# Optimization experiments

Measured on AMD Instinct MI355X. Metric: run time of the kernel, lower is better.

## Reference

```python
import jax, jax.numpy as jnp
import numpy as np

HEADS = 8
DIM = 512
DH = DIM // HEADS          # 64
M = DIM // 2               # 256 landmarks
PINV_ITERS = 6
KER = 33                   # residual depthwise conv kernel size
EPS_LN = 1e-5


def setup_inputs() -> dict:
    key = jax.random.key(0)
    ks = jax.random.split(key, 5)
    b, n, d = 4, 8192, DIM
    inner = HEADS * DH
    x = jax.random.normal(ks[0], (b, n, d), jnp.float32)
    gamma = jnp.ones((d,), jnp.float32)
    beta = jnp.zeros((d,), jnp.float32)
    w_qkv = jax.random.normal(ks[1], (d, inner * 3), jnp.float32) * (d ** -0.5)
    res_kernel = jax.random.normal(ks[2], (HEADS, 1, KER, 1), jnp.float32) * 0.1  # depthwise (groups=heads)
    w_out = jax.random.normal(ks[3], (inner, d), jnp.float32) * (inner ** -0.5)
    b_out = jnp.zeros((d,), jnp.float32)
    return dict(x=x, gamma=gamma, beta=beta, w_qkv=w_qkv,
                res_kernel=res_kernel, w_out=w_out, b_out=b_out)


def _moore_penrose_pinv(x, iters=PINV_ITERS):
    # iterative Moore-Penrose pseudo-inverse (Razavi et al.), matches lucidrains impl
    I = jnp.eye(x.shape[-1], dtype=x.dtype)
    denom = jnp.max(jnp.sum(jnp.abs(x), axis=-1)) * jnp.max(jnp.sum(jnp.abs(x), axis=-2))
    z = jnp.swapaxes(x, -1, -2) / denom
    for _ in range(iters):
        xz = x @ z
        z = 0.25 * z @ (13.0 * I - xz @ (15.0 * I - xz @ (7.0 * I - xz)))
    return z


def _forward(x, gamma, beta, w_qkv, res_kernel, w_out, b_out):
    b, n, d = x.shape
    # pre-norm (LayerNorm)
    mu = jnp.mean(x, axis=-1, keepdims=True)
    var = jnp.var(x, axis=-1, keepdims=True)
    normed = (x - mu) / jnp.sqrt(var + EPS_LN) * gamma + beta
    # left-pad so sequence divisible by num_landmarks (static, 0 here)
    pad = (-n) % M
    xp = jnp.pad(normed, ((0, 0), (pad, 0), (0, 0)))
    N = n + pad
    qkv = xp @ w_qkv                                    # [b,N,3*h*dh]
    q, k, v = jnp.split(qkv, 3, axis=-1)
    to_heads = lambda t: t.reshape(b, N, HEADS, DH).transpose(0, 2, 1, 3)  # [b,h,N,dh]
    q = to_heads(q) * (DH ** -0.5)
    k = to_heads(k)
    v = to_heads(v)
    l = N // M
    q_l = q.reshape(b, HEADS, M, l, DH).mean(axis=3)    # [b,h,m,dh] landmarks
    k_l = k.reshape(b, HEADS, M, l, DH).mean(axis=3)
    attn1 = jax.nn.softmax(jnp.einsum('bhnd,bhmd->bhnm', q, k_l), axis=-1)   # [b,h,N,m]
    attn2 = jax.nn.softmax(jnp.einsum('bhmd,bhld->bhml', q_l, k_l), axis=-1) # [b,h,m,m]
    attn3 = jax.nn.softmax(jnp.einsum('bhmd,bhnd->bhmn', q_l, k), axis=-1)   # [b,h,m,N]
    out = attn1 @ (_moore_penrose_pinv(attn2) @ (attn3 @ v))                 # [b,h,N,dh]
    # depthwise conv residual over v (channels = heads)
    conv = jax.lax.conv_general_dilated(
        v, res_kernel, window_strides=(1, 1),
        padding=((KER // 2, KER // 2), (0, 0)),
        feature_group_count=HEADS,
        dimension_numbers=('NCHW', 'OIHW', 'NCHW'))
    out = out + conv
    out = out.transpose(0, 2, 1, 3).reshape(b, N, HEADS * DH)
    out = out @ w_out + b_out                           # to_out (dropout = identity at eval)
    out = out[:, -n:]                                   # drop left padding
    return x + out                                      # TransLayer residual


def reference(x, gamma, beta, w_qkv, res_kernel, w_out, b_out):
    return _forward(x, gamma, beta, w_qkv, res_kernel, w_out, b_out)
```

## Files before the change

kernel.cpp:

```cpp
#include <hip/hip_runtime.h>
#include <hip/hip_bf16.h>

#define B_ 4
#define N_ 8192
#define D_ 512
#define H_ 8
#define DH_ 64
#define M_ 256
#define LCH 32
#define KER_ 33
#define NSPLIT 16
#define CS (N_/NSPLIT)

typedef __hip_bfloat16 bf16;
typedef __attribute__((ext_vector_type(8))) short short8;
typedef __attribute__((ext_vector_type(4))) short short4v;
typedef __attribute__((ext_vector_type(4))) float f32x4;

__device__ __forceinline__ float bf2f(bf16 h){ return __bfloat162float(h); }
__device__ __forceinline__ bf16 f2bf(float f){ return __float2bfloat16(f); }
__device__ __forceinline__ f32x4 mfma16(short8 a, short8 b, f32x4 c){
  return __builtin_amdgcn_mfma_f32_16x16x32_bf16(a, b, c, 0, 0, 0);
}

__global__ __launch_bounds__(256) void k_layernorm(const float* __restrict__ x,
    const float* __restrict__ gamma, const float* __restrict__ beta,
    bf16* __restrict__ xn){
  int row = blockIdx.x;
  const float* xr = x + (size_t)row * D_;
  bf16* o = xn + (size_t)row * D_;
  int t = threadIdx.x;
  float v0 = xr[t], v1 = xr[t+256];
  float s = v0+v1, ss = v0*v0 + v1*v1;
  __shared__ float sh[8];
  for (int off=32; off; off>>=1){ s += __shfl_xor(s,off); ss += __shfl_xor(ss,off); }
  int lane = t&63, wid = t>>6;
  if (lane==0){ sh[wid] = s; sh[wid+4] = ss; }
  __syncthreads();
  float S  = sh[0]+sh[1]+sh[2]+sh[3];
  float SS = sh[4]+sh[5]+sh[6]+sh[7];
  float mu = S*(1.f/D_);
  float var = SS*(1.f/D_) - mu*mu;
  float rs = rsqrtf(var + 1e-5f);
  o[t]     = f2bf((v0-mu)*rs*gamma[t]     + beta[t]);
  o[t+256] = f2bf((v1-mu)*rs*gamma[t+256] + beta[t+256]);
}

__global__ __launch_bounds__(256) void k_wt2(const float* __restrict__ W1, bf16* __restrict__ WT1,
    const float* __restrict__ W2, bf16* __restrict__ WT2o){
  int bx = blockIdx.x;
  const float* W; bf16* WT; int C, cx;
  if (bx < 24){ W = W1; WT = WT1; C = 1536; cx = bx; }
  else        { W = W2; WT = WT2o; C = 512;  cx = bx - 24; }
  int c0 = cx*64, r0 = blockIdx.y*64;
  __shared__ float tile[64][65];
  int t = threadIdx.x;
  for (int i=t;i<4096;i+=256){ int r=i>>6, c=i&63; tile[r][c] = W[(size_t)(r0+r)*C + c0+c]; }
  __syncthreads();
  for (int i=t;i<512;i+=256){
    int c=i>>3, rg=i&7;
    short8 o;
    #pragma unroll
    for (int j=0;j<8;j++) ((bf16*)&o)[j] = f2bf(tile[rg*8+j][c]);
    *(short8*)&WT[(size_t)(c0+c)*512 + r0 + rg*8] = o;
  }
}

__global__ __launch_bounds__(256, 2) void k_mm_qkv4(const bf16* __restrict__ A, const bf16* __restrict__ WT,
    bf16* __restrict__ qbuf, bf16* __restrict__ kbuf, bf16* __restrict__ vbuf,
    bf16* __restrict__ vT, bf16* __restrict__ qlb, bf16* __restrict__ klb){
  __shared__ __align__(16) bf16 smem[3*128*72];
  bf16 (*As)[72]  = (bf16(*)[72])smem;
  bf16 (*Bs0)[72] = (bf16(*)[72])(smem + 128*72);
  bf16 (*Bs1)[72] = (bf16(*)[72])(smem + 2*128*72);
  bf16 (*ebuf)[136] = (bf16(*)[136])smem;
  int t = threadIdx.x;
  int w = t>>6, lane = t&63, qd = lane>>4, n = lane&15;
  int wm = w>>1, wn = w&1;
  int r0 = blockIdx.y*128, c0 = blockIdx.x*256;
  f32x4 acc[2][4][4];
  #pragma unroll
  for (int cb=0;cb<2;cb++)
    #pragma unroll
    for (int i=0;i<4;i++)
      #pragma unroll
      for (int j=0;j<4;j++) acc[cb][i][j] = (f32x4){0.f,0.f,0.f,0.f};
  int srow = t>>3, skc = t&7;
  for (int k0=0; k0<512; k0+=64){
    #pragma unroll
    for (int ch=0; ch<4; ch++){
      int m = ch*32 + srow;
      *(short8*)&As[m][skc*8]  = *(const short8*)&A [(size_t)(r0+m)*512 + k0 + skc*8];
      *(short8*)&Bs0[m][skc*8] = *(const short8*)&WT[(size_t)(c0+m)*512 + k0 + skc*8];
      *(short8*)&Bs1[m][skc*8] = *(const short8*)&WT[(size_t)(c0+128+m)*512 + k0 + skc*8];
    }
    __syncthreads();
    #pragma unroll
    for (int ksub=0; ksub<2; ksub++){
      short8 af[4];
      #pragma unroll
      for (int i=0;i<4;i++) af[i] = *(const short8*)&As[wm*64+i*16+n][ksub*32+qd*8];
      #pragma unroll
      for (int cb=0; cb<2; cb++){
        bf16 (*Bsc)[72] = cb ? Bs1 : Bs0;
        short8 bfr[4];
        #pragma unroll
        for (int j=0;j<4;j++) bfr[j] = *(const short8*)&Bsc[wn*64+j*16+n][ksub*32+qd*8];
        #pragma unroll
        for (int i=0;i<4;i++)
          #pragma unroll
          for (int j=0;j<4;j++) acc[cb][i][j] = mfma16(af[i], bfr[j], acc[cb][i][j]);
      }
    }
    __syncthreads();
  }
  int part = c0 >> 9;
  bf16* dst = (part==0)? qbuf : (part==1)? kbuf : vbuf;
  float scale = (part==0)? 0.125f : 1.f;
  int b = r0 >> 13, nn = r0 & 8191;
  #pragma unroll
  for (int cb=0; cb<2; cb++){
    __syncthreads();
    #pragma unroll
    for (int i=0;i<4;i++)
      #pragma unroll
      for (int j=0;j<4;j++)
        #pragma unroll
        for (int rg=0; rg<4; rg++)
          ebuf[wm*64+i*16+qd*4+rg][wn*64+j*16+n] = f2bf(acc[cb][i][j][rg]*scale);
    __syncthreads();
    #pragma unroll
    for (int rep=0; rep<8; rep++){
      int unit = rep*256 + t;
      int row = unit >> 4, ch = unit & 15;
      int col = c0 + cb*128 + ch*8;
      int cc = col & 511, h = cc>>6, dh = cc&63;
      *(short8*)&dst[(((size_t)(b*H_+h))*N_ + nn + row)*DH_ + dh] = *(const short8*)&ebuf[row][ch*8];
    }
    if (part < 2){
      bf16* lt = (part==0) ? qlb : klb;
      #pragma unroll
      for (int rep=0; rep<2; rep++){
        int oi = rep*256 + t;
        int chunk = oi >> 7, col = oi & 127;
        float sum = 0.f;
        #pragma unroll
        for (int rr=0; rr<32; rr++) sum += bf2f(ebuf[chunk*32+rr][col]);
        int m = (nn >> 5) + chunk;
        int cc = (c0 + cb*128 + col) & 511;
        int h = cc >> 6, dh = cc & 63;
        lt[(((size_t)(b*H_+h))*M_ + m)*DH_ + dh] = f2bf(sum * (1.f/LCH));
      }
    } else {
      __syncthreads();
      #pragma unroll
      for (int i=0;i<4;i++)
        #pragma unroll
        for (int j=0;j<4;j++){
          short4v tv;
          #pragma unroll
          for (int rg=0; rg<4; rg++) ((bf16*)&tv)[rg] = f2bf(acc[cb][i][j][rg]);
          *(short4v*)&ebuf[wn*64+j*16+n][wm*64+i*16+qd*4] = tv;
        }
      __syncthreads();
      #pragma unroll
      for (int rep=0; rep<8; rep++){
        int unit = rep*256 + t;
        int col = unit >> 4, ch = unit & 15;
        int cc = (c0 + cb*128 + col) & 511;
        int h = cc >> 6, dh = cc & 63;
        *(short8*)&vT[(((size_t)(b*H_+h))*DH_ + dh)*N_ + nn + ch*8] = *(const short8*)&ebuf[col][ch*8];
      }
    }
  }
}

__global__ __launch_bounds__(256) void k_attn2(const bf16* __restrict__ ql, const bf16* __restrict__ kl,
    float* __restrict__ A2, bf16* __restrict__ A2b){
  int bhm = blockIdx.x;
  int bh = bhm >> 8, m = bhm & 255;
  int t = threadIdx.x;
  __shared__ float qrow[64];
  __shared__ float sh[4];
  if (t < 64) qrow[t] = bf2f(ql[((size_t)bh*M_ + m)*DH_ + t]);
  __syncthreads();
  const bf16* krow = kl + ((size_t)bh*M_ + t)*DH_;
  float s = 0.f;
  #pragma unroll
  for (int i=0;i<64;i++) s += qrow[i]*bf2f(krow[i]);
  float e = __expf(s);
  float sum = e;
  for (int off=32; off; off>>=1) sum += __shfl_xor(sum, off);
  if ((t&63)==0) sh[t>>6] = sum;
  __syncthreads();
  sum = sh[0]+sh[1]+sh[2]+sh[3];
  float r = e/sum;
  A2[((size_t)bh*M_ + m)*M_ + t] = r;
  A2b[((size_t)bh*M_ + m)*M_ + t] = f2bf(r);
}

__global__ __launch_bounds__(256) void k_pinv_init(const float* __restrict__ A2, bf16* __restrict__ Z){
  int bh = blockIdx.x;
  int t = threadIdx.x;
  const float* Ab = A2 + (size_t)bh*M_*M_;
  bf16* Zb = Z + (size_t)bh*M_*M_;
  float cs=0.f;
  for (int r=0;r<M_;r++) cs += Ab[(size_t)r*M_ + t];
  __shared__ float sh[4];
  float v = cs;
  for (int off=32; off; off>>=1) v = fmaxf(v, __shfl_xor(v, off));
  if ((t&63)==0) sh[t>>6] = v;
  __syncthreads();
  float maxc = fmaxf(fmaxf(sh[0],sh[1]), fmaxf(sh[2],sh[3]));
  float inv = 1.f/maxc;
  for (int r=0;r<M_;r++) Zb[(size_t)r*M_ + t] = f2bf(Ab[(size_t)t*M_ + r]*inv);
}

__global__ __launch_bounds__(256) void k_gemm_pmb(bf16* __restrict__ C, const bf16* __restrict__ A,
    const bf16* __restrict__ Bm, float bDiag, int bNeg, float cDiag, int cNeg, float cScale){
  int bh = blockIdx.y;
  int tm = blockIdx.x >> 2, tn = blockIdx.x & 3;
  const bf16* Ab = A  + (size_t)bh*65536;
  const bf16* Bb = Bm + (size_t)bh*65536;
  bf16* Cb = C + (size_t)bh*65536;
  __shared__ __align__(16) bf16 Ah[64][136];
  __shared__ __align__(16) bf16 Bh[64][136];
  int t = threadIdx.x;
  int w = t>>6, lane = t&63, qd = lane>>4, n = lane&15;
  int wm = w>>1, wn = w&1;
  int r0 = tm*64, c0 = tn*64;
  f32x4 acc[2][2];
  #pragma unroll
  for (int i=0;i<2;i++)
    #pragma unroll
    for (int j=0;j<2;j++) acc[i][j] = (f32x4){0.f,0.f,0.f,0.f};
  int arow = t>>2, akc = (t&3)*32;
  int bkrow = t>>1, bcc = (t&1)*32;
  for (int k0=0; k0<256; k0+=128){
    #pragma unroll
    for (int vv=0; vv<4; vv++)
      *(short8*)&Ah[arow][akc+vv*8] = *(const short8*)&Ab[(size_t)(r0+arow)*256 + k0+akc+vv*8];
    int kr = k0 + bkrow;
    #pragma unroll
    for (int vv=0; vv<4; vv++){
      short8 vb = *(const short8*)&Bb[(size_t)kr*256 + c0 + bcc + vv*8];
      if (bNeg){
        #pragma unroll
        for (int j=0;j<8;j++){
          float x = (kr == (c0 + bcc + vv*8 + j) ? bDiag : 0.f) - bf2f(((bf16*)&vb)[j]);
          Bh[bcc+vv*8+j][bkrow] = f2bf(x);
        }
      } else {
        #pragma unroll
        for (int j=0;j<8;j++) Bh[bcc+vv*8+j][bkrow] = ((bf16*)&vb)[j];
      }
    }
    __syncthreads();
    #pragma unroll
    for (int ksub=0; ksub<4; ksub++){
      short8 afh[2], bfh[2];
      #pragma unroll
      for (int i=0;i<2;i++) afh[i] = *(const short8*)&Ah[wm*32+i*16+n][ksub*32+qd*8];
      #pragma unroll
      for (int j=0;j<2;j++) bfh[j] = *(const short8*)&Bh[wn*32+j*16+n][ksub*32+qd*8];
      #pragma unroll
      for (int i=0;i<2;i++)
        #pragma unroll
        for (int j=0;j<2;j++) acc[i][j] = mfma16(afh[i], bfh[j], acc[i][j]);
    }
    __syncthreads();
  }
  #pragma unroll
  for (int i=0;i<2;i++){
    #pragma unroll
    for (int j=0;j<2;j++){
      int cidx = c0 + wn*32 + j*16 + n;
      #pragma unroll
      for (int rg=0; rg<4; rg++){
        int r = r0 + wm*32 + i*16 + qd*4 + rg;
        float r_ = acc[i][j][rg];
        if (cNeg) r_ = ((r==cidx)? cDiag : 0.f) - r_;
        Cb[(size_t)r*256 + cidx] = f2bf(r_*cScale);
      }
    }
  }
}

__global__ __launch_bounds__(256) void k_gemm_pm(float* __restrict__ C, const void* __restrict__ Av,
    const void* __restrict__ Bv, float bDiag, int bNeg, float cDiag, int cNeg, float cScale,
    int aBf, int bBf){
  int bh = blockIdx.y;
  int tm = blockIdx.x >> 2, tn = blockIdx.x & 3;
  const float* Af = (const float*)Av; const bf16* A16 = (const bf16*)Av;
  const float* Bf = (const float*)Bv; const bf16* B16 = (const bf16*)Bv;
  float* Cb = C + (size_t)bh*65536;
  __shared__ __align__(16) bf16 Ah[64][72];
  __shared__ __align__(16) bf16 Al[64][72];
  __shared__ __align__(16) bf16 Bh[64][72];
  __shared__ __align__(16) bf16 Bl[64][72];
  int t = threadIdx.x;
  int w = t>>6, lane = t&63, qd = lane>>4, n = lane&15;
  int wm = w>>1, wn = w&1;
  int r0 = tm*64, c0 = tn*64;
  f32x4 acc[2][2];
  #pragma unroll
  for (int i=0;i<2;i++)
    #pragma unroll
    for (int j=0;j<2;j++) acc[i][j] = (f32x4){0.f,0.f,0.f,0.f};
  int srow = t>>3, skc = t&7;
  for (int k0=0; k0<256; k0+=64){
    #pragma unroll
    for (int ch=0; ch<2; ch++){
      int m = ch*32 + srow;
      if (aBf){
        *(short8*)&Ah[m][skc*8] = *(const short8*)&A16[(size_t)bh*65536 + (size_t)(r0+m)*256 + k0 + skc*8];
      } else {
        short8 vh, vl;
        const float* ap = &Af[(size_t)bh*65536 + (size_t)(r0+m)*256 + k0 + skc*8];
        #pragma unroll
        for (int j=0;j<8;j++){
          float x = ap[j];
          bf16 h = f2bf(x);
          ((bf16*)&vh)[j] = h;
          ((bf16*)&vl)[j] = f2bf(x - bf2f(h));
        }
        *(short8*)&Ah[m][skc*8] = vh;
        *(short8*)&Al[m][skc*8] = vl;
      }
      int kr = k0 + m;
      if (bBf){
        short8 vb = *(const short8*)&B16[(size_t)bh*65536 + (size_t)(k0+m)*256 + c0 + skc*8];
        #pragma unroll
        for (int j=0;j<8;j++) Bh[skc*8+j][m] = ((bf16*)&vb)[j];
      } else {
        const float* bp = &Bf[(size_t)bh*65536 + (size_t)(k0+m)*256 + c0 + skc*8];
        #pragma unroll
        for (int j=0;j<8;j++){
          float x = bp[j];
          if (bNeg) x = (kr == (c0 + skc*8 + j) ? bDiag : 0.f) - x;
          bf16 h = f2bf(x);
          Bh[skc*8+j][m] = h;
          Bl[skc*8+j][m] = f2bf(x - bf2f(h));
        }
      }
    }
    __syncthreads();
    #pragma unroll
    for (int ksub=0; ksub<2; ksub++){
      short8 afh[2], afl[2], bfh[2], bfl[2];
      #pragma unroll
      for (int i=0;i<2;i++){
        afh[i] = *(const short8*)&Ah[wm*32+i*16+n][ksub*32+qd*8];
        if (!aBf) afl[i] = *(const short8*)&Al[wm*32+i*16+n][ksub*32+qd*8];
      }
      #pragma unroll
      for (int j=0;j<2;j++){
        bfh[j] = *(const short8*)&Bh[wn*32+j*16+n][ksub*32+qd*8];
        if (!bBf) bfl[j] = *(const short8*)&Bl[wn*32+j*16+n][ksub*32+qd*8];
      }
      #pragma unroll
      for (int i=0;i<2;i++)
        #pragma unroll
        for (int j=0;j<2;j++){
          if (!aBf) acc[i][j] = mfma16(afl[i], bfh[j], acc[i][j]);
          if (!bBf) acc[i][j] = mfma16(afh[i], bfl[j], acc[i][j]);
          acc[i][j] = mfma16(afh[i], bfh[j], acc[i][j]);
        }
    }
    __syncthreads();
  }
  #pragma unroll
  for (int i=0;i<2;i++){
    #pragma unroll
    for (int j=0;j<2;j++){
      int cidx = c0 + wn*32 + j*16 + n;
      #pragma unroll
      for (int rg=0; rg<4; rg++){
        int r = r0 + wm*32 + i*16 + qd*4 + rg;
        float r_ = acc[i][j][rg];
        if (cNeg) r_ = ((r==cidx)? cDiag : 0.f) - r_;
        Cb[(size_t)r*256 + cidx] = r_*cScale;
      }
    }
  }
}

__global__ __launch_bounds__(256) void k_gemm_z2(bf16* __restrict__ z2t, const float* __restrict__ A,
    const bf16* __restrict__ Bm){
  int bh = blockIdx.y;
  int tm = blockIdx.x;
  const float* Ab = A  + (size_t)bh*65536;
  const bf16* Bb = Bm + (size_t)bh*M_*DH_;
  __shared__ float As[16][68];
  __shared__ float Bs[16][64];
  int t = threadIdx.x, tx = t&15, ty = t>>4;
  int r0 = tm*64;
  float acc[4][4] = {};
  for (int k0=0;k0<256;k0+=16){
    for (int i=t;i<1024;i+=256){
      int m=i>>4, kq=i&15;
      As[kq][m] = Ab[(size_t)(r0+m)*256 + k0+kq];
      int nn=i&63, k2=i>>6;
      Bs[k2][nn] = bf2f(Bb[(size_t)(k0+k2)*64 + nn]);
    }
    __syncthreads();
    #pragma unroll
    for (int kq=0;kq<16;kq++){
      float a0[4], b0[4];
      #pragma unroll
      for (int i=0;i<4;i++) a0[i] = As[kq][ty*4+i];
      #pragma unroll
      for (int j=0;j<4;j++) b0[j] = Bs[kq][tx*4+j];
      #pragma unroll
      for (int i=0;i<4;i++)
        #pragma unroll
        for (int j=0;j<4;j++) acc[i][j] += a0[i]*b0[j];
    }
    __syncthreads();
  }
  #pragma unroll
  for (int i=0;i<4;i++){
    int r = r0+ty*4+i;
    #pragma unroll
    for (int j=0;j<4;j++)
      z2t[(size_t)bh*16384 + (size_t)(tx*4+j)*256 + r] = f2bf(acc[i][j]);
  }
}

__global__ __launch_bounds__(256, 2) void k_flash_split(const bf16* __restrict__ Q,
    const bf16* __restrict__ K, const bf16* __restrict__ VT,
    float* __restrict__ OP, float* __restrict__ LP){
  int bh = blockIdx.y;
  int sp = blockIdx.x;
  int t = threadIdx.x, w = t>>6, lane = t&63, qd = lane>>4, n = lane&15;
  int r0 = w*64;
  const size_t Qoff = ((size_t)bh*M_ + r0)*DH_;
  const size_t Koff = ((size_t)bh*N_ + (size_t)sp*CS)*DH_;
  const size_t Voff = (size_t)bh*DH_*N_ + (size_t)sp*CS;
  __shared__ __align__(16) bf16 pbuf[4][4][16][72];
  short8 aq[4][2];
  #pragma unroll
  for (int rt=0; rt<4; rt++){
    aq[rt][0] = *(const short8*)&Q[Qoff + (size_t)(rt*16+n)*DH_ + qd*8];
    aq[rt][1] = *(const short8*)&Q[Qoff + (size_t)(rt*16+n)*DH_ + 32 + qd*8];
  }
  f32x4 o[4][4];
  float lrun[4][4];
  #pragma unroll
  for (int rt=0; rt<4; rt++){
    #pragma unroll
    for (int j=0;j<4;j++){ o[rt][j] = (f32x4){0.f,0.f,0.f,0.f}; lrun[rt][j] = 0.f; }
  }
  for (int tl=0; tl<CS/64; ++tl){
    const bf16* kp = K + Koff + (size_t)(tl*64)*DH_;
    short8 kb[4][2];
    #pragma unroll
    for (int cg=0; cg<4; cg++){
      kb[cg][0] = *(const short8*)&kp[(size_t)(cg*16+n)*DH_ + qd*8];
      kb[cg][1] = *(const short8*)&kp[(size_t)(cg*16+n)*DH_ + 32 + qd*8];
    }
    #pragma unroll
    for (int rt=0; rt<4; rt++){
      f32x4 s[4];
      #pragma unroll
      for (int cg=0; cg<4; cg++){
        f32x4 z = (f32x4){0.f,0.f,0.f,0.f};
        z = mfma16(aq[rt][0], kb[cg][0], z);
        z = mfma16(aq[rt][1], kb[cg][1], z);
        s[cg] = z;
      }
      #pragma unroll
      for (int rg=0; rg<4; rg++){
        float p0 = __expf(s[0][rg]), p1 = __expf(s[1][rg]);
        float p2 = __expf(s[2][rg]), p3 = __expf(s[3][rg]);
        float ts = p0+p1+p2+p3;
        ts += __shfl_xor(ts,1); ts += __shfl_xor(ts,2);
        ts += __shfl_xor(ts,4); ts += __shfl_xor(ts,8);
        lrun[rt][rg] += ts;
        pbuf[w][rt][qd*4+rg][n]    = f2bf(p0);
        pbuf[w][rt][qd*4+rg][16+n] = f2bf(p1);
        pbuf[w][rt][qd*4+rg][32+n] = f2bf(p2);
        pbuf[w][rt][qd*4+rg][48+n] = f2bf(p3);
      }
    }
    const bf16* vp = VT + Voff + tl*64 + qd*8;
    short8 vb[4][2];
    #pragma unroll
    for (int dg=0; dg<4; dg++){
      vb[dg][0] = *(const short8*)&vp[(size_t)(dg*16+n)*N_];
      vb[dg][1] = *(const short8*)&vp[(size_t)(dg*16+n)*N_ + 32];
    }
    #pragma unroll
    for (int rt=0; rt<4; rt++){
      short8 ap0 = *(const short8*)&pbuf[w][rt][n][qd*8];
      short8 ap1 = *(const short8*)&pbuf[w][rt][n][32+qd*8];
      #pragma unroll
      for (int dg=0; dg<4; dg++){
        o[rt][dg] = mfma16(ap0, vb[dg][0], o[rt][dg]);
        o[rt][dg] = mfma16(ap1, vb[dg][1], o[rt][dg]);
      }
    }
  }
  size_t base = ((size_t)sp*(B_*H_) + bh)*M_;
  #pragma unroll
  for (int rt=0; rt<4; rt++){
    #pragma unroll
    for (int rg=0; rg<4; rg++){
      int row = r0 + rt*16 + qd*4 + rg;
      if (n==0) LP[base+row] = lrun[rt][rg];
      #pragma unroll
      for (int dg=0; dg<4; dg++)
        OP[(base+row)*DH_ + dg*16 + n] = o[rt][dg][rg];
    }
  }
}

__global__ __launch_bounds__(256) void k_flash_merge(const float* __restrict__ OP,
    const float* __restrict__ LP, bf16* __restrict__ O){
  int bh = blockIdx.y;
  int r = blockIdx.x*4 + (threadIdx.x>>6);
  int dh = threadIdx.x & 63;
  float acc = 0.f, den = 0.f;
  for (int s=0; s<NSPLIT; s++){
    size_t base = ((size_t)s*(B_*H_) + bh)*M_ + r;
    den += LP[base];
    acc += OP[base*DH_ + dh];
  }
  O[((size_t)bh*M_ + r)*DH_ + dh] = f2bf(acc/den);
}

__global__ __launch_bounds__(256, 2) void k_flash_w3(const bf16* __restrict__ Q,
    const bf16* __restrict__ K, const bf16* __restrict__ VT, bf16* __restrict__ O){
  int bh = blockIdx.y;
  int t = threadIdx.x, w = t>>6, lane = t&63, qd = lane>>4, n = lane&15;
  int r0 = blockIdx.x*256 + w*64;
  const size_t Qoff = ((size_t)bh*N_ + r0)*DH_;
  const size_t Koff = (size_t)bh*M_*DH_;
  const size_t Voff = (size_t)bh*DH_*M_;
  __shared__ __align__(16) bf16 pbuf[4][4][16][72];
  short8 aq[4][2];
  #pragma unroll
  for (int rt=0; rt<4; rt++){
    aq[rt][0] = *(const short8*)&Q[Qoff + (size_t)(rt*16+n)*DH_ + qd*8];
    aq[rt][1] = *(const short8*)&Q[Qoff + (size_t)(rt*16+n)*DH_ + 32 + qd*8];
  }
  f32x4 o[4][4];
  float lrun[4][4];
  #pragma unroll
  for (int rt=0; rt<4; rt++){
    #pragma unroll
    for (int j=0;j<4;j++){ o[rt][j] = (f32x4){0.f,0.f,0.f,0.f}; lrun[rt][j] = 0.f; }
  }
  #pragma unroll
  for (int tl=0; tl<4; ++tl){
    const bf16* kp = K + Koff + (size_t)(tl*64)*DH_;
    short8 kb[4][2];
    #pragma unroll
    for (int cg=0; cg<4; cg++){
      kb[cg][0] = *(const short8*)&kp[(size_t)(cg*16+n)*DH_ + qd*8];
      kb[cg][1] = *(const short8*)&kp[(size_t)(cg*16+n)*DH_ + 32 + qd*8];
    }
    #pragma unroll
    for (int rt=0; rt<4; rt++){
      f32x4 s[4];
      #pragma unroll
      for (int cg=0; cg<4; cg++){
        f32x4 z = (f32x4){0.f,0.f,0.f,0.f};
        z = mfma16(aq[rt][0], kb[cg][0], z);
        z = mfma16(aq[rt][1], kb[cg][1], z);
        s[cg] = z;
      }
      #pragma unroll
      for (int rg=0; rg<4; rg++){
        float p0 = __expf(s[0][rg]), p1 = __expf(s[1][rg]);
        float p2 = __expf(s[2][rg]), p3 = __expf(s[3][rg]);
        float ts = p0+p1+p2+p3;
        ts += __shfl_xor(ts,1); ts += __shfl_xor(ts,2);
        ts += __shfl_xor(ts,4); ts += __shfl_xor(ts,8);
        lrun[rt][rg] += ts;
        pbuf[w][rt][qd*4+rg][n]    = f2bf(p0);
        pbuf[w][rt][qd*4+rg][16+n] = f2bf(p1);
        pbuf[w][rt][qd*4+rg][32+n] = f2bf(p2);
        pbuf[w][rt][qd*4+rg][48+n] = f2bf(p3);
      }
    }
    const bf16* vp = VT + Voff + tl*64 + qd*8;
    short8 vb[4][2];
    #pragma unroll
    for (int dg=0; dg<4; dg++){
      vb[dg][0] = *(const short8*)&vp[(size_t)(dg*16+n)*M_];
      vb[dg][1] = *(const short8*)&vp[(size_t)(dg*16+n)*M_ + 32];
    }
    #pragma unroll
    for (int rt=0; rt<4; rt++){
      short8 ap0 = *(const short8*)&pbuf[w][rt][n][qd*8];
      short8 ap1 = *(const short8*)&pbuf[w][rt][n][32+qd*8];
      #pragma unroll
      for (int dg=0; dg<4; dg++){
        o[rt][dg] = mfma16(ap0, vb[dg][0], o[rt][dg]);
        o[rt][dg] = mfma16(ap1, vb[dg][1], o[rt][dg]);
      }
    }
  }
  #pragma unroll
  for (int rt=0; rt<4; rt++){
    #pragma unroll
    for (int rg=0; rg<4; rg++){
      float inv = 1.f/lrun[rt][rg];
      size_t rowoff = ((size_t)bh*N_ + r0 + rt*16 + qd*4 + rg)*DH_;
      #pragma unroll
      for (int dg=0; dg<4; dg++)
        O[rowoff + dg*16 + n] = f2bf(o[rt][dg][rg]*inv);
    }
  }
}

#define CCH 128
__global__ __launch_bounds__(256, 4) void k_conv_add(const bf16* __restrict__ v, const float* __restrict__ w,
    bf16* __restrict__ outh){
  int bh = blockIdx.y;
  int n0 = blockIdx.x * CCH;
  int h = bh & 7;
  __shared__ bf16 vs[CCH+32][72];
  __shared__ float wk[KER_];
  int t = threadIdx.x;
  if (t < KER_) wk[t] = w[h*KER_ + t];
  const bf16* vb = v + (size_t)bh*N_*DH_;
  for (int i=t; i<(CCH+32)*8; i+=256){
    int r = i>>3, cg = i&7;
    int nn = n0 - 16 + r;
    short8 val = {0,0,0,0,0,0,0,0};
    if (nn >= 0 && nn < N_) val = *(const short8*)&vb[(size_t)nn*DH_ + cg*8];
    *(short8*)&vs[r][cg*8] = val;
  }
  __syncthreads();
  int dhg = t & 7, rowg = t >> 3;
  bf16* ob = outh + ((size_t)bh*N_ + n0)*DH_;
  #pragma unroll
  for (int rr=0; rr<4; rr++){
    int lr = rowg*4 + rr;
    short8 o = *(short8*)&ob[(size_t)lr*DH_ + dhg*8];
    float acc[8] = {0.f,0.f,0.f,0.f,0.f,0.f,0.f,0.f};
    #pragma unroll 3
    for (int tt=0; tt<KER_; tt++){
      short8 vv = *(const short8*)&vs[lr+tt][dhg*8];
      float wt = wk[tt];
      #pragma unroll
      for (int j=0;j<8;j++) acc[j] += wt * bf2f(((bf16*)&vv)[j]);
    }
    #pragma unroll
    for (int j=0;j<8;j++) ((bf16*)&o)[j] = f2bf(bf2f(((bf16*)&o)[j]) + acc[j]);
    *(short8*)&ob[(size_t)lr*DH_ + dhg*8] = o;
  }
}

__global__ __launch_bounds__(256) void k_mm_out2(const bf16* __restrict__ Ahd, const bf16* __restrict__ WT2,
    const float* __restrict__ bias, const float* __restrict__ xin, float* __restrict__ out){
  __shared__ __align__(16) bf16 As[128][72];
  __shared__ __align__(16) bf16 Bs[128][72];
  int t = threadIdx.x;
  int w = t>>6, lane = t&63, qd = lane>>4, n = lane&15;
  int wm = w>>1, wn = w&1;
  int bid = blockIdx.x;
  int xcd = bid & 7, pos = bid >> 3;
  int tid = xcd*128 + pos;
  int cx = tid & 3, ry = tid >> 2;
  int r0 = ry*128, c0 = cx*128;
  f32x4 acc[4][4];
  #pragma unroll
  for (int i=0;i<4;i++)
    #pragma unroll
    for (int j=0;j<4;j++) acc[i][j] = (f32x4){0.f,0.f,0.f,0.f};
  int srow = t>>3, skc = t&7;
  for (int k0=0; k0<512; k0+=64){
    int h = k0 >> 6;
    #pragma unroll
    for (int ch=0; ch<4; ch++){
      int m = ch*32 + srow;
      int r = r0 + m, b = r>>13, nn = r&8191;
      *(short8*)&As[m][skc*8] = *(const short8*)&Ahd[((size_t)(b*H_+h)*N_ + nn)*DH_ + skc*8];
      *(short8*)&Bs[m][skc*8] = *(const short8*)&WT2[(size_t)(c0+m)*512 + k0 + skc*8];
    }
    __syncthreads();
    #pragma unroll
    for (int ksub=0; ksub<2; ksub++){
      short8 af[4], bfr[4];
      #pragma unroll
      for (int i=0;i<4;i++) af[i]  = *(const short8*)&As[wm*64+i*16+n][ksub*32+qd*8];
      #pragma unroll
      for (int j=0;j<4;j++) bfr[j] = *(const short8*)&Bs[wn*64+j*16+n][ksub*32+qd*8];
      #pragma unroll
      for (int i=0;i<4;i++)
        #pragma unroll
        for (int j=0;j<4;j++) acc[i][j] = mfma16(af[i], bfr[j], acc[i][j]);
    }
    __syncthreads();
  }
  #pragma unroll
  for (int i=0;i<4;i++){
    #pragma unroll
    for (int rg=0; rg<4; rg++){
      int r = r0 + wm*64 + i*16 + qd*4 + rg;
      size_t base = (size_t)r*512;
      #pragma unroll
      for (int j=0;j<4;j++){
        int c = c0 + wn*64 + j*16 + n;
        out[base + c] = acc[i][j][rg] + bias[c] + xin[base + c];
      }
    }
  }
}

extern "C" void kernel_launch(void* const* d_in, const int* in_sizes, int n_in,
                              void* d_out, int out_size, void* d_ws, size_t ws_size,
                              hipStream_t stream) {
  const float* x     = (const float*)d_in[0];
  const float* gamma = (const float*)d_in[1];
  const float* beta  = (const float*)d_in[2];
  const float* wqkv  = (const float*)d_in[3];
  const float* resk  = (const float*)d_in[4];
  const float* wout  = (const float*)d_in[5];
  const float* bout  = (const float*)d_in[6];
  float* out = (float*)d_out;

  const size_t SL = (size_t)B_*H_*N_*DH_;
  const size_t SM = (size_t)B_*H_*M_*DH_;
  const size_t SP = (size_t)B_*H_*M_*M_;

  bf16* xn  = (bf16*)d_ws;
  bf16* q   = xn + SL;
  bf16* k   = q + SL;
  bf16* v   = k + SL;
  bf16* vT  = v + SL;
  bf16* ql  = vT + SL;
  bf16* kl  = ql + SM;
  bf16* kv3 = kl + SM;
  bf16* z2T = kv3 + SM;
  float* A2 = (float*)(z2T + SM);
  bf16* WT  = (bf16*)(A2 + SP);
  bf16* WT2 = WT + (size_t)1536*512;
  float* P1 = (float*)xn;
  float* P2 = P1 + SP;
  float* P3 = P2 + SP;
  float* P4 = P3 + SP;
  float* OPp = (float*)xn;
  float* LPp = (float*)z2T;
  bf16* A2b = k;
  bf16* Zb0 = A2b + SP;
  bf16* Zb1 = Zb0 + SP;
  bf16* Pb  = Zb1 + SP;
  bf16* Tb  = Pb + SP;
  bf16* Ub  = Tb + SP;

  k_wt2<<<dim3(32, 8), 256, 0, stream>>>(wqkv, WT, wout, WT2);
  k_layernorm<<<B_*N_, 256, 0, stream>>>(x, gamma, beta, xn);
  k_mm_qkv4<<<dim3(6, 256), 256, 0, stream>>>(xn, WT, q, k, v, vT, ql, kl);

  k_flash_split<<<dim3(NSPLIT, B_*H_), 256, 0, stream>>>(ql, k, vT, OPp, LPp);
  k_flash_merge<<<dim3(M_/4, B_*H_), 256, 0, stream>>>(OPp, LPp, kv3);

  k_attn2<<<B_*H_*M_, 256, 0, stream>>>(ql, kl, A2, A2b);
  k_pinv_init<<<B_*H_, 256, 0, stream>>>(A2, Zb0);

  bf16* Zbi = Zb0; bf16* Zbo = Zb1;
  for (int it=0; it<5; ++it){
    k_gemm_pmb<<<dim3(16,32), 256, 0, stream>>>(Pb,  A2b, Zbi, 0.f,0, 0.f,0, 1.f);
    k_gemm_pmb<<<dim3(16,32), 256, 0, stream>>>(Tb,  Pb,  Pb,  7.f,1, 15.f,1, 1.f);
    k_gemm_pmb<<<dim3(16,32), 256, 0, stream>>>(Ub,  Pb,  Tb,  0.f,0, 13.f,1, 1.f);
    k_gemm_pmb<<<dim3(16,32), 256, 0, stream>>>(Zbo, Zbi, Ub,  0.f,0, 0.f,0, 0.25f);
    bf16* tt = Zbi; Zbi = Zbo; Zbo = tt;
  }
  k_gemm_pm<<<dim3(16,32), 256, 0, stream>>>(P2, A2, Zbi, 0.f,0, 0.f,0, 1.f,  0,1);
  k_gemm_pm<<<dim3(16,32), 256, 0, stream>>>(P3, P2, P2,  7.f,1, 15.f,1, 1.f, 0,0);
  k_gemm_pm<<<dim3(16,32), 256, 0, stream>>>(P4, P2, P3,  0.f,0, 13.f,1, 1.f, 0,0);
  k_gemm_pm<<<dim3(16,32), 256, 0, stream>>>(P1, Zbi, P4, 0.f,0, 0.f,0, 0.25f,1,0);

  k_gemm_z2<<<dim3(4, B_*H_), 256, 0, stream>>>(z2T, P1, kv3);
  k_flash_w3<<<dim3(N_/256, B_*H_), 256, 0, stream>>>(q, kl, z2T, xn);
  k_conv_add<<<dim3(N_/CCH, B_*H_), 256, 0, stream>>>(v, resk, xn);
  k_mm_out2<<<1024, 256, 0, stream>>>(xn, WT2, bout, x, out);
}
```

Baseline: 704.8 us.

## Fuse depthwise conv residual into attention output kernel; use direct global-to-LDS loads in QKV GEMM

The depthwise conv residual is folded into the flash_w3 epilogue. The attention output tile is staged in LDS (reusing pbuf), the conv is added there, and the result is written once, so the separate conv kernel and its read-modify-write of xn go away. Separately, the QKV GEMM now loads A and W tiles with global_load_lds and uses an XOR-swizzled unpadded LDS layout, which drops the register round-trip and avoids bank conflicts. The larger LDS footprint in flash_w3 (a 288x72 v tile) may reduce occupancy.

```diff
diff --git a/kernel.cpp b/kernel.cpp
--- a/kernel.cpp
+++ b/kernel.cpp
@@ -21,6 +21,10 @@
 __device__ __forceinline__ bf16 f2bf(float f){ return __float2bfloat16(f); }
 __device__ __forceinline__ f32x4 mfma16(short8 a, short8 b, f32x4 c){
   return __builtin_amdgcn_mfma_f32_16x16x32_bf16(a, b, c, 0, 0, 0);
+}
+__device__ __forceinline__ void gload_lds16(const bf16* g, bf16* l){
+  __builtin_amdgcn_global_load_lds((const __attribute__((address_space(1))) void*)g,
+                                   (__attribute__((address_space(3))) void*)l, 16, 0, 0);
 }
 
 __global__ __launch_bounds__(256) void k_layernorm(const float* __restrict__ x,
@@ -69,15 +73,18 @@
 __global__ __launch_bounds__(256, 2) void k_mm_qkv4(const bf16* __restrict__ A, const bf16* __restrict__ WT,
     bf16* __restrict__ qbuf, bf16* __restrict__ kbuf, bf16* __restrict__ vbuf,
     bf16* __restrict__ vT, bf16* __restrict__ qlb, bf16* __restrict__ klb){
-  __shared__ __align__(16) bf16 smem[3*128*72];
-  bf16 (*As)[72]  = (bf16(*)[72])smem;
-  bf16 (*Bs0)[72] = (bf16(*)[72])(smem + 128*72);
-  bf16 (*Bs1)[72] = (bf16(*)[72])(smem + 2*128*72);
+  __shared__ __align__(16) bf16 smem[3*128*64];
+  bf16 (*As)[64]  = (bf16(*)[64])smem;
+  bf16 (*Bs0)[64] = (bf16(*)[64])(smem + 128*64);
+  bf16 (*Bs1)[64] = (bf16(*)[64])(smem + 2*128*64);
   bf16 (*ebuf)[136] = (bf16(*)[136])smem;
   int t = threadIdx.x;
   int w = t>>6, lane = t&63, qd = lane>>4, n = lane&15;
   int wm = w>>1, wn = w&1;
   int r0 = blockIdx.y*128, c0 = blockIdx.x*256;
+  int lrow = w*8 + (lane>>3);
+  int csw  = ((lane&7) ^ (lane>>3)) * 8;
+  int xA = (n&7)*8;
   f32x4 acc[2][4][4];
   #pragma unroll
   for (int cb=0;cb<2;cb++)
@@ -85,27 +92,27 @@
     for (int i=0;i<4;i++)
       #pragma unroll
       for (int j=0;j<4;j++) acc[cb][i][j] = (f32x4){0.f,0.f,0.f,0.f};
-  int srow = t>>3, skc = t&7;
   for (int k0=0; k0<512; k0+=64){
     #pragma unroll
     for (int ch=0; ch<4; ch++){
-      int m = ch*32 + srow;
-      *(short8*)&As[m][skc*8]  = *(const short8*)&A [(size_t)(r0+m)*512 + k0 + skc*8];
-      *(short8*)&Bs0[m][skc*8] = *(const short8*)&WT[(size_t)(c0+m)*512 + k0 + skc*8];
-      *(short8*)&Bs1[m][skc*8] = *(const short8*)&WT[(size_t)(c0+128+m)*512 + k0 + skc*8];
+      int m = ch*32 + lrow;
+      gload_lds16(&A [(size_t)(r0+m)*512 + k0 + csw], &As[ch*32 + w*8][0]);
+      gload_lds16(&WT[(size_t)(c0+m)*512 + k0 + csw], &Bs0[ch*32 + w*8][0]);
+      gload_lds16(&WT[(size_t)(c0+128+m)*512 + k0 + csw], &Bs1[ch*32 + w*8][0]);
     }
     __syncthreads();
     #pragma unroll
     for (int ksub=0; ksub<2; ksub++){
+      int colE = (ksub*32 + qd*8) ^ xA;
       short8 af[4];
       #pragma unroll
-      for (int i=0;i<4;i++) af[i] = *(const short8*)&As[wm*64+i*16+n][ksub*32+qd*8];
+      for (int i=0;i<4;i++) af[i] = *(const short8*)&As[wm*64+i*16+n][colE];
       #pragma unroll
       for (int cb=0; cb<2; cb++){
-        bf16 (*Bsc)[72] = cb ? Bs1 : Bs0;
+        bf16 (*Bsc)[64] = cb ? Bs1 : Bs0;
         short8 bfr[4];
         #pragma unroll
-        for (int j=0;j<4;j++) bfr[j] = *(const short8*)&Bsc[wn*64+j*16+n][ksub*32+qd*8];
+        for (int j=0;j<4;j++) bfr[j] = *(const short8*)&Bsc[wn*64+j*16+n][colE];
         #pragma unroll
         for (int i=0;i<4;i++)
           #pragma unroll
@@ -530,14 +537,30 @@
 }
 
 __global__ __launch_bounds__(256, 2) void k_flash_w3(const bf16* __restrict__ Q,
-    const bf16* __restrict__ K, const bf16* __restrict__ VT, bf16* __restrict__ O){
+    const bf16* __restrict__ K, const bf16* __restrict__ VT,
+    const bf16* __restrict__ v, const float* __restrict__ wconv, bf16* __restrict__ O){
   int bh = blockIdx.y;
   int t = threadIdx.x, w = t>>6, lane = t&63, qd = lane>>4, n = lane&15;
-  int r0 = blockIdx.x*256 + w*64;
+  int R0 = blockIdx.x*256;
+  int r0 = R0 + w*64;
+  int h = bh & 7;
   const size_t Qoff = ((size_t)bh*N_ + r0)*DH_;
   const size_t Koff = (size_t)bh*M_*DH_;
   const size_t Voff = (size_t)bh*DH_*M_;
   __shared__ __align__(16) bf16 pbuf[4][4][16][72];
+  __shared__ __align__(16) bf16 vtile[288][72];
+  __shared__ float wk[KER_];
+  if (t < KER_) wk[t] = wconv[h*KER_ + t];
+  {
+    const bf16* vb = v + (size_t)bh*N_*DH_;
+    for (int i=t; i<288*8; i+=256){
+      int r = i>>3, cg = i&7;
+      int nn = R0 - 16 + r;
+      short8 val = {0,0,0,0,0,0,0,0};
+      if (nn >= 0 && nn < N_) val = *(const short8*)&vb[(size_t)nn*DH_ + cg*8];
+      *(short8*)&vtile[r][cg*8] = val;
+    }
+  }
   short8 aq[4][2];
   #pragma unroll
   for (int rt=0; rt<4; rt++){
@@ -602,55 +625,37 @@
       }
     }
   }
+  bf16 (*obuf)[72] = (bf16(*)[72])pbuf;
   #pragma unroll
   for (int rt=0; rt<4; rt++){
     #pragma unroll
     for (int rg=0; rg<4; rg++){
       float inv = 1.f/lrun[rt][rg];
-      size_t rowoff = ((size_t)bh*N_ + r0 + rt*16 + qd*4 + rg)*DH_;
+      int row = w*64 + rt*16 + qd*4 + rg;
       #pragma unroll
       for (int dg=0; dg<4; dg++)
-        O[rowoff + dg*16 + n] = f2bf(o[rt][dg][rg]*inv);
-    }
-  }
-}
-
-#define CCH 128
-__global__ __launch_bounds__(256, 4) void k_conv_add(const bf16* __restrict__ v, const float* __restrict__ w,
-    bf16* __restrict__ outh){
-  int bh = blockIdx.y;
-  int n0 = blockIdx.x * CCH;
-  int h = bh & 7;
-  __shared__ bf16 vs[CCH+32][72];
-  __shared__ float wk[KER_];
-  int t = threadIdx.x;
-  if (t < KER_) wk[t] = w[h*KER_ + t];
-  const bf16* vb = v + (size_t)bh*N_*DH_;
-  for (int i=t; i<(CCH+32)*8; i+=256){
-    int r = i>>3, cg = i&7;
-    int nn = n0 - 16 + r;
-    short8 val = {0,0,0,0,0,0,0,0};
-    if (nn >= 0 && nn < N_) val = *(const short8*)&vb[(size_t)nn*DH_ + cg*8];
-    *(short8*)&vs[r][cg*8] = val;
+        obuf[row][dg*16 + n] = f2bf(o[rt][dg][rg]*inv);
+    }
   }
   __syncthreads();
   int dhg = t & 7, rowg = t >> 3;
-  bf16* ob = outh + ((size_t)bh*N_ + n0)*DH_;
-  #pragma unroll
-  for (int rr=0; rr<4; rr++){
-    int lr = rowg*4 + rr;
-    short8 o = *(short8*)&ob[(size_t)lr*DH_ + dhg*8];
+  bf16* ob = O + ((size_t)bh*N_ + R0)*DH_;
+  #pragma unroll
+  for (int rr=0; rr<8; rr++){
+    int lr = rowg*8 + rr;
     float acc[8] = {0.f,0.f,0.f,0.f,0.f,0.f,0.f,0.f};
     #pragma unroll 3
     for (int tt=0; tt<KER_; tt++){
-      short8 vv = *(const short8*)&vs[lr+tt][dhg*8];
+      short8 vv = *(const short8*)&vtile[lr+tt][dhg*8];
       float wt = wk[tt];
       #pragma unroll
       for (int j=0;j<8;j++) acc[j] += wt * bf2f(((bf16*)&vv)[j]);
     }
-    #pragma unroll
-    for (int j=0;j<8;j++) ((bf16*)&o)[j] = f2bf(bf2f(((bf16*)&o)[j]) + acc[j]);
-    *(short8*)&ob[(size_t)lr*DH_ + dhg*8] = o;
+    short8 ao = *(const short8*)&obuf[lr][dhg*8];
+    short8 oo;
+    #pragma unroll
+    for (int j=0;j<8;j++) ((bf16*)&oo)[j] = f2bf(bf2f(((bf16*)&ao)[j]) + acc[j]);
+    *(short8*)&ob[(size_t)lr*DH_ + dhg*8] = oo;
   }
 }
 
@@ -776,7 +781,6 @@
   k_gemm_pm<<<dim3(16,32), 256, 0, stream>>>(P1, Zbi, P4, 0.f,0, 0.f,0, 0.25f,1,0);
 
   k_gemm_z2<<<dim3(4, B_*H_), 256, 0, stream>>>(z2T, P1, kv3);
-  k_flash_w3<<<dim3(N_/256, B_*H_), 256, 0, stream>>>(q, kl, z2T, xn);
-  k_conv_add<<<dim3(N_/CCH, B_*H_), 256, 0, stream>>>(v, resk, xn);
+  k_flash_w3<<<dim3(N_/256, B_*H_), 256, 0, stream>>>(q, kl, z2T, v, resk, xn);
   k_mm_out2<<<1024, 256, 0, stream>>>(xn, WT2, bout, x, out);
 }
```

New measurement: 675.4 us. -4.2%, faster.
